# Kernel optimization log

Hardware: AMD Instinct MI355X
Metric: run time of the kernel (lower is better)

Reference implementation:

```python
import jax, jax.numpy as jnp
import numpy as np

B, L, NMOD = 200, 50, 3          # dialogues, uniform dialogue length, modalities (l,a,v)
N_DIM, NHIDDEN, NUM_K, NSPK = 128, 128, 4, 2
NN = B * NMOD * L                # total graph nodes = 30000


def _build_edge_index():
    # within-modality full permutations per dialogue
    idx = np.arange(L)
    u, v = np.meshgrid(idx, idx, indexing='ij')
    m = u != v
    pw = np.stack([u[m], v[m]])                                    # [2, L*(L-1)]
    offs = (np.arange(B)[:, None] * NMOD * L + np.arange(NMOD)[None, :] * L).reshape(-1)
    within = (pw[None, :, :] + offs[:, None, None]).transpose(1, 0, 2).reshape(2, -1)
    # cross-modal permutations of (l_t, a_t, v_t) per utterance
    mo = np.arange(NMOD) * L
    mu, mv = np.meshgrid(mo, mo, indexing='ij')
    mm = mu != mv
    pc = np.stack([mu[mm], mv[mm]])                                # [2, 6]
    offs2 = (np.arange(B)[:, None] * NMOD * L + np.arange(L)[None, :]).reshape(-1)
    cross = (pc[None, :, :] + offs2[:, None, None]).transpose(1, 0, 2).reshape(2, -1)
    return np.concatenate([within, cross], axis=1).astype(np.int32)  # [2, 1530000]


def setup_inputs():
    key = jax.random.key(0)
    ks = jax.random.split(key, 6)
    a = jax.random.normal(ks[0], (B * L, N_DIM), jnp.float32)
    v = jax.random.normal(ks[1], (B * L, N_DIM), jnp.float32)
    l = jax.random.normal(ks[2], (B * L, N_DIM), jnp.float32)
    qmask = jax.random.uniform(ks[3], (L, B, NSPK), jnp.float32)
    W1 = jax.random.normal(ks[4], (NHIDDEN, N_DIM), jnp.float32) / np.sqrt(N_DIM)
    b1 = jnp.zeros((NHIDDEN,), jnp.float32)
    speaker_emb = jax.random.normal(ks[5], (NSPK, N_DIM), jnp.float32)
    kappas = jnp.ones((NUM_K,), jnp.float32)
    edge_index = jnp.asarray(_build_edge_index())
    return {"a": a, "v": v, "l": l, "qmask": qmask, "W1": W1, "b1": b1,
            "speaker_emb": speaker_emb, "kappas": kappas,
            "edge_index": edge_index, "epoch": 0}


def _hgcn_block(x, src, dst, inv_deg, kappa):
    # gather-aggregate-scatter hypergraph conv: mean over incoming edges, kappa-weighted residual
    agg = jax.ops.segment_sum(x[src], dst, num_segments=NN) * inv_deg
    return jax.nn.relu(x + kappa * agg)


def reference(a, v, l, qmask, W1, b1, speaker_emb, kappas, edge_index, epoch):
    # flatten qmask per dialogue (uniform lengths) -> speaker id per utterance
    spk_idx = jnp.argmax(qmask.transpose(1, 0, 2).reshape(B * L, NSPK), axis=-1)
    l = l + speaker_emb[spk_idx]                    # use_speaker and 'l' in modals
    # per-dialogue node ordering: [l_b; a_b; v_b]
    feats = jnp.concatenate([l.reshape(B, L, N_DIM),
                             a.reshape(B, L, N_DIM),
                             v.reshape(B, L, N_DIM)], axis=1).reshape(NN, N_DIM)
    x = feats @ W1.T + b1
    src, dst = edge_index[0], edge_index[1]
    deg = jax.ops.segment_sum(jnp.ones((src.shape[0],), jnp.float32), dst, num_segments=NN)
    inv_deg = (1.0 / jnp.maximum(deg, 1.0))[:, None]
    for k in range(NUM_K):
        x = _hgcn_block(x, src, dst, inv_deg, kappas[k])
    x = jnp.concatenate([feats, x], axis=-1)        # use_residue
    D = x.shape[-1]
    xr = x.reshape(B, NMOD, L, D)
    # reverse_features: cat l/a/v feature blocks along last dim, utterance-major
    out = jnp.concatenate([xr[:, 0], xr[:, 1], xr[:, 2]], axis=-1).reshape(B * L, NMOD * D)
    return out
```

## Files before the change

kernel.cpp:

```cpp
#include <hip/hip_runtime.h>

#define NB   200
#define LL   50
#define ND   128

typedef __attribute__((ext_vector_type(8))) short bf16x8;
typedef __attribute__((ext_vector_type(4))) float f32x4;

#define FS   136
#define SMEM_BYTES (192 * FS * 2)

__device__ __forceinline__ short f2bf(float x) {
    unsigned u = __float_as_uint(x);
    return (short)((u + 0x7fffu + ((u >> 16) & 1u)) >> 16);
}

__device__ __forceinline__ float bf2f(short h) {
    return __uint_as_float(((unsigned)(unsigned short)h) << 16);
}

__device__ __forceinline__ bf16x8 pack8(f32x4 lo, f32x4 hi) {
    bf16x8 r;
    r[0] = f2bf(lo[0]); r[1] = f2bf(lo[1]); r[2] = f2bf(lo[2]); r[3] = f2bf(lo[3]);
    r[4] = f2bf(hi[0]); r[5] = f2bf(hi[1]); r[6] = f2bf(hi[2]); r[7] = f2bf(hi[3]);
    return r;
}

__launch_bounds__(512, 2)
__global__ void hgcn_fused(const float* __restrict__ a,
                           const float* __restrict__ v,
                           const float* __restrict__ l,
                           const float* __restrict__ qmask,
                           const float* __restrict__ W1,
                           const float* __restrict__ b1,
                           const float* __restrict__ se,
                           const float* __restrict__ kap,
                           float* __restrict__ out) {
    extern __shared__ char smem[];
    short* featsB = (short*)smem;

    const int b    = blockIdx.x;
    const int tid  = threadIdx.x;
    const int lane = tid & 63;
    const int w    = tid >> 6;
    const int r    = lane & 15;
    const int q    = lane >> 4;
    const int d    = 16 * w + r;

    const f32x4* a4  = (const f32x4*)a;
    const f32x4* v4  = (const f32x4*)v;
    const f32x4* l4  = (const f32x4*)l;
    const f32x4* se4 = (const f32x4*)se;
    const f32x4* W14 = (const f32x4*)W1;
    f32x4* out4 = (f32x4*)out;

    const f32x4 kap4 = *(const f32x4*)kap;
    const float bias = b1[d];
    bf16x8 wfr[4];
    #pragma unroll
    for (int ks = 0; ks < 4; ++ks) {
        f32x4 g0 = W14[(16 * w + r) * 32 + ks * 8 + q * 2];
        f32x4 g1 = W14[(16 * w + r) * 32 + ks * 8 + q * 2 + 1];
        wfr[ks] = pack8(g0, g1);
    }

    for (int i = tid; i < 3072; i += 512) {
        int prow = i >> 4, c8 = i & 15;
        int m = prow >> 6, t = prow & 63;
        f32x4 f0 = {0.f, 0.f, 0.f, 0.f}, f1 = {0.f, 0.f, 0.f, 0.f};
        if (t < LL) {
            const f32x4* src = (m == 0) ? l4 : ((m == 1) ? a4 : v4);
            int base = (b * LL + t) * 32 + c8 * 2;
            f0 = src[base]; f1 = src[base + 1];
            if (m == 0) {
                int qb  = (t * NB + b) * 2;
                int spk = qmask[qb + 1] > qmask[qb] ? 1 : 0;
                f0 += se4[spk * 32 + c8 * 2];
                f1 += se4[spk * 32 + c8 * 2 + 1];
            }
        }
        *(bf16x8*)&featsB[prow * FS + c8 * 8] = pack8(f0, f1);
    }
    __syncthreads();

    f32x4 acc[12];
    #pragma unroll
    for (int nt = 0; nt < 12; ++nt) acc[nt] = (f32x4){0.f, 0.f, 0.f, 0.f};
    #pragma unroll
    for (int ks = 0; ks < 4; ++ks)
        #pragma unroll
        for (int nt = 0; nt < 12; ++nt) {
            bf16x8 af = *(const bf16x8*)&featsB[(16 * nt + r) * FS + ks * 32 + q * 8];
            acc[nt] = __builtin_amdgcn_mfma_f32_16x16x32_bf16(af, wfr[ks], acc[nt], 0, 0, 0);
        }

    for (int i = tid; i < 3072; i += 512) {
        int prow = i >> 4, c8 = i & 15;
        int m = prow >> 6, t = prow & 63;
        if (t < LL) {
            bf16x8 hv = *(const bf16x8*)&featsB[prow * FS + c8 * 8];
            f32x4 f0, f1;
            f0[0] = bf2f(hv[0]); f0[1] = bf2f(hv[1]); f0[2] = bf2f(hv[2]); f0[3] = bf2f(hv[3]);
            f1[0] = bf2f(hv[4]); f1[1] = bf2f(hv[5]); f1[2] = bf2f(hv[6]); f1[3] = bf2f(hv[7]);
            size_t o = (size_t)(b * LL + t) * 192 + m * 64 + c8 * 2;
            out4[o]     = f0;
            out4[o + 1] = f1;
        }
    }

    #pragma unroll
    for (int nt = 0; nt < 12; ++nt) {
        int t0 = 16 * (nt & 3) + 4 * q;
        #pragma unroll
        for (int e = 0; e < 4; ++e)
            acc[nt][e] = (t0 + e < LL) ? acc[nt][e] + bias : 0.0f;
    }

    const float inv = 1.0f / 51.0f;
    #pragma unroll
    for (int it = 0; it < 4; ++it) {
        const float f = kap4[it] * inv;
        const float g = 1.0f - 2.0f * f;
        float S[3];
        #pragma unroll
        for (int m = 0; m < 3; ++m) {
            f32x4 s4 = acc[4 * m] + acc[4 * m + 1] + acc[4 * m + 2] + acc[4 * m + 3];
            float s = s4[0] + s4[1] + s4[2] + s4[3];
            s += __shfl_xor(s, 16, 64);
            s += __shfl_xor(s, 32, 64);
            S[m] = s;
        }
        #pragma unroll
        for (int j = 0; j < 4; ++j) {
            int t0 = 16 * j + 4 * q;
            #pragma unroll
            for (int e = 0; e < 4; ++e) {
                float c = acc[j][e] + acc[4 + j][e] + acc[8 + j][e];
                bool valid = (t0 + e) < LL;
                #pragma unroll
                for (int m = 0; m < 3; ++m) {
                    float xv = acc[4 * m + j][e];
                    float nv = fmaxf(fmaf(f, S[m] + c, g * xv), 0.0f);
                    acc[4 * m + j][e] = valid ? nv : 0.0f;
                }
            }
        }
    }

    const size_t ob = (size_t)b * LL * 768 + 128 + d;
    #pragma unroll
    for (int m = 0; m < 3; ++m)
        #pragma unroll
        for (int j = 0; j < 4; ++j) {
            int t0 = 16 * j + 4 * q;
            #pragma unroll
            for (int e = 0; e < 4; ++e) {
                int t = t0 + e;
                if (t < LL)
                    out[ob + (size_t)t * 768 + m * 256] = acc[4 * m + j][e];
            }
        }
}

extern "C" void kernel_launch(void* const* d_in, const int* in_sizes, int n_in,
                              void* d_out, int out_size, void* d_ws, size_t ws_size,
                              hipStream_t stream) {
    const float* a     = (const float*)d_in[0];
    const float* v     = (const float*)d_in[1];
    const float* l     = (const float*)d_in[2];
    const float* qmask = (const float*)d_in[3];
    const float* W1    = (const float*)d_in[4];
    const float* b1    = (const float*)d_in[5];
    const float* se    = (const float*)d_in[6];
    const float* kap   = (const float*)d_in[7];
    float* out = (float*)d_out;

    hipFuncSetAttribute((const void*)hgcn_fused,
                        hipFuncAttributeMaxDynamicSharedMemorySize, SMEM_BYTES);
    hgcn_fused<<<NB, 512, SMEM_BYTES, stream>>>(a, v, l, qmask, W1, b1, se, kap, out);
}
```

Baseline: 20.91 us.

## Warp-specialize block: extra 512 threads write residue features during MFMA compute

The block grows from 512 to 1024 threads and splits by role. The first 512 threads do the bf16 MFMA projection and the four propagation steps. The other 512 threads read the raw fp32 inputs (plus the speaker embedding) and write the residue half of the output. The goal is to overlap the residue stores with the matrix and propagation work instead of running them one after the other. The cost is extra global reads of the inputs, and the tighter launch bounds may limit registers and cause spills; as a side effect the residue is written from fp32 inputs instead of bf16-rounded values.

Result: faster. 17.93 us (-14.2%).

```diff
diff --git a/kernel.cpp b/kernel.cpp
--- a/kernel.cpp
+++ b/kernel.cpp
@@ -15,10 +15,6 @@
     return (short)((u + 0x7fffu + ((u >> 16) & 1u)) >> 16);
 }
 
-__device__ __forceinline__ float bf2f(short h) {
-    return __uint_as_float(((unsigned)(unsigned short)h) << 16);
-}
-
 __device__ __forceinline__ bf16x8 pack8(f32x4 lo, f32x4 hi) {
     bf16x8 r;
     r[0] = f2bf(lo[0]); r[1] = f2bf(lo[1]); r[2] = f2bf(lo[2]); r[3] = f2bf(lo[3]);
@@ -26,7 +22,7 @@
     return r;
 }
 
-__launch_bounds__(512, 2)
+__launch_bounds__(1024, 4)
 __global__ void hgcn_fused(const float* __restrict__ a,
                            const float* __restrict__ v,
                            const float* __restrict__ l,
@@ -45,7 +41,6 @@
     const int w    = tid >> 6;
     const int r    = lane & 15;
     const int q    = lane >> 4;
-    const int d    = 16 * w + r;
 
     const f32x4* a4  = (const f32x4*)a;
     const f32x4* v4  = (const f32x4*)v;
@@ -54,17 +49,22 @@
     const f32x4* W14 = (const f32x4*)W1;
     f32x4* out4 = (f32x4*)out;
 
-    const f32x4 kap4 = *(const f32x4*)kap;
-    const float bias = b1[d];
+    f32x4 kap4 = {0.f, 0.f, 0.f, 0.f};
+    float bias = 0.0f;
     bf16x8 wfr[4];
-    #pragma unroll
-    for (int ks = 0; ks < 4; ++ks) {
-        f32x4 g0 = W14[(16 * w + r) * 32 + ks * 8 + q * 2];
-        f32x4 g1 = W14[(16 * w + r) * 32 + ks * 8 + q * 2 + 1];
-        wfr[ks] = pack8(g0, g1);
+    const int d = 16 * w + r;
+    if (tid < 512) {
+        kap4 = *(const f32x4*)kap;
+        bias = b1[d];
+        #pragma unroll
+        for (int ks = 0; ks < 4; ++ks) {
+            f32x4 g0 = W14[d * 32 + ks * 8 + q * 2];
+            f32x4 g1 = W14[d * 32 + ks * 8 + q * 2 + 1];
+            wfr[ks] = pack8(g0, g1);
+        }
     }
 
-    for (int i = tid; i < 3072; i += 512) {
+    for (int i = tid; i < 3072; i += 1024) {
         int prow = i >> 4, c8 = i & 15;
         int m = prow >> 6, t = prow & 63;
         f32x4 f0 = {0.f, 0.f, 0.f, 0.f}, f1 = {0.f, 0.f, 0.f, 0.f};
@@ -83,83 +83,89 @@
     }
     __syncthreads();
 
-    f32x4 acc[12];
-    #pragma unroll
-    for (int nt = 0; nt < 12; ++nt) acc[nt] = (f32x4){0.f, 0.f, 0.f, 0.f};
-    #pragma unroll
-    for (int ks = 0; ks < 4; ++ks)
+    if (tid < 512) {
+        f32x4 acc[12];
+        #pragma unroll
+        for (int nt = 0; nt < 12; ++nt) acc[nt] = (f32x4){0.f, 0.f, 0.f, 0.f};
+        #pragma unroll
+        for (int ks = 0; ks < 4; ++ks)
+            #pragma unroll
+            for (int nt = 0; nt < 12; ++nt) {
+                bf16x8 af = *(const bf16x8*)&featsB[(16 * nt + r) * FS + ks * 32 + q * 8];
+                acc[nt] = __builtin_amdgcn_mfma_f32_16x16x32_bf16(af, wfr[ks], acc[nt], 0, 0, 0);
+            }
+
         #pragma unroll
         for (int nt = 0; nt < 12; ++nt) {
-            bf16x8 af = *(const bf16x8*)&featsB[(16 * nt + r) * FS + ks * 32 + q * 8];
-            acc[nt] = __builtin_amdgcn_mfma_f32_16x16x32_bf16(af, wfr[ks], acc[nt], 0, 0, 0);
+            int t0 = 16 * (nt & 3) + 4 * q;
+            #pragma unroll
+            for (int e = 0; e < 4; ++e)
+                acc[nt][e] = (t0 + e < LL) ? acc[nt][e] + bias : 0.0f;
         }
 
-    for (int i = tid; i < 3072; i += 512) {
-        int prow = i >> 4, c8 = i & 15;
-        int m = prow >> 6, t = prow & 63;
-        if (t < LL) {
-            bf16x8 hv = *(const bf16x8*)&featsB[prow * FS + c8 * 8];
-            f32x4 f0, f1;
-            f0[0] = bf2f(hv[0]); f0[1] = bf2f(hv[1]); f0[2] = bf2f(hv[2]); f0[3] = bf2f(hv[3]);
-            f1[0] = bf2f(hv[4]); f1[1] = bf2f(hv[5]); f1[2] = bf2f(hv[6]); f1[3] = bf2f(hv[7]);
+        const float inv = 1.0f / 51.0f;
+        #pragma unroll
+        for (int it = 0; it < 4; ++it) {
+            const float f = kap4[it] * inv;
+            const float g = 1.0f - 2.0f * f;
+            float S[3];
+            #pragma unroll
+            for (int m = 0; m < 3; ++m) {
+                f32x4 s4 = acc[4 * m] + acc[4 * m + 1] + acc[4 * m + 2] + acc[4 * m + 3];
+                float s = s4[0] + s4[1] + s4[2] + s4[3];
+                s += __shfl_xor(s, 16, 64);
+                s += __shfl_xor(s, 32, 64);
+                S[m] = s;
+            }
+            #pragma unroll
+            for (int j = 0; j < 4; ++j) {
+                int t0 = 16 * j + 4 * q;
+                #pragma unroll
+                for (int e = 0; e < 4; ++e) {
+                    float c = acc[j][e] + acc[4 + j][e] + acc[8 + j][e];
+                    bool valid = (t0 + e) < LL;
+                    #pragma unroll
+                    for (int m = 0; m < 3; ++m) {
+                        float xv = acc[4 * m + j][e];
+                        float nv = fmaxf(fmaf(f, S[m] + c, g * xv), 0.0f);
+                        acc[4 * m + j][e] = valid ? nv : 0.0f;
+                    }
+                }
+            }
+        }
+
+        const size_t ob = (size_t)b * LL * 768 + 128 + d;
+        #pragma unroll
+        for (int m = 0; m < 3; ++m)
+            #pragma unroll
+            for (int j = 0; j < 4; ++j) {
+                int t0 = 16 * j + 4 * q;
+                #pragma unroll
+                for (int e = 0; e < 4; ++e) {
+                    int t = t0 + e;
+                    if (t < LL)
+                        out[ob + (size_t)t * 768 + m * 256] = acc[4 * m + j][e];
+                }
+            }
+    } else {
+        for (int i = tid - 512; i < 2400; i += 512) {
+            int row = i >> 4, c8 = i & 15;
+            int m = row >= 100 ? 2 : (row >= 50 ? 1 : 0);
+            int t = row - m * 50;
+            const f32x4* src = (m == 0) ? l4 : ((m == 1) ? a4 : v4);
+            int base = (b * LL + t) * 32 + c8 * 2;
+            f32x4 f0 = src[base], f1 = src[base + 1];
+            if (m == 0) {
+                int qb  = (t * NB + b) * 2;
+                int spk = qmask[qb + 1] > qmask[qb] ? 1 : 0;
+                f0 += se4[spk * 32 + c8 * 2];
+                f1 += se4[spk * 32 + c8 * 2 + 1];
+            }
             size_t o = (size_t)(b * LL + t) * 192 + m * 64 + c8 * 2;
             out4[o]     = f0;
             out4[o + 1] = f1;
         }
     }
-
-    #pragma unroll
-    for (int nt = 0; nt < 12; ++nt) {
-        int t0 = 16 * (nt & 3) + 4 * q;
-        #pragma unroll
-        for (int e = 0; e < 4; ++e)
-            acc[nt][e] = (t0 + e < LL) ? acc[nt][e] + bias : 0.0f;
-    }
-
-    const float inv = 1.0f / 51.0f;
-    #pragma unroll
-    for (int it = 0; it < 4; ++it) {
-        const float f = kap4[it] * inv;
-        const float g = 1.0f - 2.0f * f;
-        float S[3];
-        #pragma unroll
-        for (int m = 0; m < 3; ++m) {
-            f32x4 s4 = acc[4 * m] + acc[4 * m + 1] + acc[4 * m + 2] + acc[4 * m + 3];
-            float s = s4[0] + s4[1] + s4[2] + s4[3];
-            s += __shfl_xor(s, 16, 64);
-            s += __shfl_xor(s, 32, 64);
-            S[m] = s;
-        }
-        #pragma unroll
-        for (int j = 0; j < 4; ++j) {
-            int t0 = 16 * j + 4 * q;
-            #pragma unroll
-            for (int e = 0; e < 4; ++e) {
-                float c = acc[j][e] + acc[4 + j][e] + acc[8 + j][e];
-                bool valid = (t0 + e) < LL;
-                #pragma unroll
-                for (int m = 0; m < 3; ++m) {
-                    float xv = acc[4 * m + j][e];
-                    float nv = fmaxf(fmaf(f, S[m] + c, g * xv), 0.0f);
-                    acc[4 * m + j][e] = valid ? nv : 0.0f;
-                }
-            }
-        }
-    }
-
-    const size_t ob = (size_t)b * LL * 768 + 128 + d;
-    #pragma unroll
-    for (int m = 0; m < 3; ++m)
-        #pragma unroll
-        for (int j = 0; j < 4; ++j) {
-            int t0 = 16 * j + 4 * q;
-            #pragma unroll
-            for (int e = 0; e < 4; ++e) {
-                int t = t0 + e;
-                if (t < LL)
-                    out[ob + (size_t)t * 768 + m * 256] = acc[4 * m + j][e];
-            }
-        }
 }
 
 extern "C" void kernel_launch(void* const* d_in, const int* in_sizes, int n_in,
@@ -177,5 +183,5 @@
 
     hipFuncSetAttribute((const void*)hgcn_fused,
                         hipFuncAttributeMaxDynamicSharedMemorySize, SMEM_BYTES);
-    hgcn_fused<<<NB, 512, SMEM_BYTES, stream>>>(a, v, l, qmask, W1, b1, se, kap, out);
+    hgcn_fused<<<NB, 1024, SMEM_BYTES, stream>>>(a, v, l, qmask, W1, b1, se, kap, out);
 }
```
